# Performance work log

Measured on AMD Instinct MI355X. Metric: run time of the kernel, lower is better.

## Reference

```python
import jax, jax.numpy as jnp
import numpy as np

N_NODES = 100000
N_EDGES = 1200000
D = 64
N_LAYERS = 3


def setup_inputs() -> dict:
    key = jax.random.key(0)
    k0, k1, k2, k3, k4 = jax.random.split(key, 5)
    x = jax.random.normal(k0, (N_NODES, D), dtype=jnp.float32)
    edge_index = jax.random.randint(k1, (2, N_EDGES), 0, N_NODES, dtype=jnp.int32)
    edge_weight = jax.random.uniform(k2, (N_EDGES,), dtype=jnp.float32)
    # stacked per-layer params: 3 layers of 64->64
    self_kernels = jax.random.normal(k3, (N_LAYERS, D, D), dtype=jnp.float32) * 0.1
    neighbor_kernels = jax.random.normal(k4, (N_LAYERS, D, D), dtype=jnp.float32) * 0.1
    biases = jnp.zeros((N_LAYERS, D), dtype=jnp.float32)
    return {"x": x, "edge_index": edge_index, "edge_weight": edge_weight,
            "self_kernels": self_kernels, "neighbor_kernels": neighbor_kernels,
            "biases": biases}


def _sage_layer(h, row, col, edge_weight, self_k, neigh_k, b):
    # gather source-node features per edge, weight them: [E, d]
    msg = h[col] * edge_weight[:, None]
    # sum-aggregate messages at target nodes: [N, d]
    agg = jax.ops.segment_sum(msg, row, num_segments=N_NODES)
    # concat=False -> self transform + neighbor transform added, then relu
    out = h @ self_k + agg @ neigh_k + b
    return jax.nn.relu(out)


def reference(x, edge_index, edge_weight, self_kernels, neighbor_kernels, biases):
    row, col = edge_index[0], edge_index[1]
    h = x
    for i in range(N_LAYERS):
        h = _sage_layer(h, row, col, edge_weight,
                        self_kernels[i], neighbor_kernels[i], biases[i])
    return h
```

## Files before the change

kernel.cpp:

```cpp
#include <hip/hip_runtime.h>

#define NN 100000
#define NE 1200000
#define DD 64
#define NTILES 3125
#define NBK 391
#define MLEN (NBK * 256)
#define EPB 4688

typedef unsigned int uint32;
typedef unsigned char uint8;
typedef unsigned short ushort16;
typedef __attribute__((ext_vector_type(8))) short short8;
typedef __attribute__((ext_vector_type(16))) float f32x16;

__device__ __forceinline__ ushort16 f2bf(float x) {
    uint32 u = __float_as_uint(x);
    u += 0x7FFFu + ((u >> 16) & 1u);
    return (ushort16)(u >> 16);
}
__device__ __forceinline__ float bflo(uint32 u) { return __uint_as_float(u << 16); }
__device__ __forceinline__ float bfhi(uint32 u) { return __uint_as_float(u & 0xFFFF0000u); }
__device__ __forceinline__ uint32 pack2(float a, float b) {
    return (uint32)f2bf(a) | ((uint32)f2bf(b) << 16);
}

__device__ __forceinline__ void agg_edges8(float* a, int s, int e, int fl,
                                           const uint32* __restrict__ edges,
                                           const uint4* __restrict__ y4) {
    #pragma unroll 4
    for (int j = s; j < e; j++) {
        uint32 ed = edges[j];
        int c = (int)(ed >> 15);
        float w = (float)(ed & 32767u) * (1.0f / 32767.0f);
        uint4 yv = y4[c * 8 + fl];
        a[0] = fmaf(bflo(yv.x), w, a[0]);
        a[1] = fmaf(bfhi(yv.x), w, a[1]);
        a[2] = fmaf(bflo(yv.y), w, a[2]);
        a[3] = fmaf(bfhi(yv.y), w, a[3]);
        a[4] = fmaf(bflo(yv.z), w, a[4]);
        a[5] = fmaf(bfhi(yv.z), w, a[5]);
        a[6] = fmaf(bflo(yv.w), w, a[6]);
        a[7] = fmaf(bfhi(yv.w), w, a[7]);
    }
}


__global__ __launch_bounds__(512)
void k_init(const int* __restrict__ row, int* __restrict__ M,
            const float* __restrict__ selfk, const float* __restrict__ neighk,
            short8* __restrict__ wpack) {
    if (blockIdx.x >= 256) {
        int tid = (blockIdx.x - 256) * 512 + threadIdx.x;
        if (tid < 3 * 16 * 64) {
            int lane  = tid & 63;
            int frag  = (tid >> 6) & 15;
            int layer = tid >> 10;
            int g = frag >> 3;
            int t = (frag >> 2) & 1;
            int s = frag & 3;
            const float* W = (g ? neighk : selfk) + layer * 4096;
            int n = t * 32 + (lane & 31);
            int k0 = s * 16 + (lane >> 5) * 8;
            short8 v;
            #pragma unroll
            for (int j = 0; j < 8; j++) v[j] = (short)f2bf(W[(k0 + j) * 64 + n]);
            wpack[tid] = v;
        }
        return;
    }
    __shared__ int bins[NBK];
    for (int i = threadIdx.x; i < NBK; i += 512) bins[i] = 0;
    __syncthreads();
    int start = blockIdx.x * EPB;
    int end = min(start + EPB, NE);
    for (int e = start + (int)threadIdx.x; e < end; e += 512)
        atomicAdd(&bins[row[e] >> 8], 1);
    __syncthreads();
    for (int i = threadIdx.x; i < NBK; i += 512)
        M[i * 256 + blockIdx.x] = bins[i];
}


__global__ void k_scan1(const int* __restrict__ in, int* __restrict__ outx,
                        int* __restrict__ partials) {
    __shared__ int tmp[256];
    int t = threadIdx.x;
    int i = blockIdx.x * 256 + t;
    int v = (i < MLEN) ? in[i] : 0;
    tmp[t] = v;
    __syncthreads();
    #pragma unroll
    for (int off = 1; off < 256; off <<= 1) {
        int add = (t >= off) ? tmp[t - off] : 0;
        __syncthreads();
        tmp[t] += add;
        __syncthreads();
    }
    if (i < MLEN) outx[i] = tmp[t] - v;
    if (t == 255) partials[blockIdx.x] = tmp[255];
}

__global__ void k_scan2(int* __restrict__ partials) {
    __shared__ int tmp[512];
    int t = threadIdx.x;
    int v = (t < NBK) ? partials[t] : 0;
    tmp[t] = v;
    __syncthreads();
    #pragma unroll
    for (int off = 1; off < 512; off <<= 1) {
        int add = (t >= off) ? tmp[t - off] : 0;
        __syncthreads();
        tmp[t] += add;
        __syncthreads();
    }
    if (t < NBK) partials[t] = tmp[t] - v;
}

__global__ __launch_bounds__(512)
void k_bscatter(const int* __restrict__ row, const int* __restrict__ col,
                const float* __restrict__ ew, const int* __restrict__ Mscan,
                const int* __restrict__ partials,
                uint32* __restrict__ colw, uint8* __restrict__ rowlo) {
    __shared__ int cur[NBK];
    for (int i = threadIdx.x; i < NBK; i += 512)
        cur[i] = Mscan[i * 256 + blockIdx.x] + partials[i];
    __syncthreads();
    int start = blockIdx.x * EPB;
    int end = min(start + EPB, NE);
    for (int e = start + (int)threadIdx.x; e < end; e += 512) {
        int r = row[e];
        int wq = (int)(ew[e] * 32767.0f + 0.5f);
        wq = (wq > 32767) ? 32767 : wq;
        int p = atomicAdd(&cur[r >> 8], 1);
        colw[p]  = ((uint32)col[e] << 15) | (uint32)wq;
        rowlo[p] = (uint8)(r & 255);
    }
}

__global__ __launch_bounds__(256)
void k_build(const int* __restrict__ Mscan, const int* __restrict__ partials,
             const uint32* __restrict__ colw, const uint8* __restrict__ rowlo,
             uint32* __restrict__ edges, int* __restrict__ offsets) {
    __shared__ int bins[256];
    __shared__ int tmp[256];
    __shared__ int cur[256];
    int b = blockIdx.x;
    int t = threadIdx.x;
    int bstart = Mscan[b * 256] + partials[b];
    int bend   = (b == NBK - 1) ? NE : Mscan[(b + 1) * 256] + partials[b + 1];
    bins[t] = 0;
    __syncthreads();
    for (int p = bstart + t; p < bend; p += 256)
        atomicAdd(&bins[rowlo[p]], 1);
    __syncthreads();
    int v = bins[t];
    tmp[t] = v;
    __syncthreads();
    #pragma unroll
    for (int off = 1; off < 256; off <<= 1) {
        int add = (t >= off) ? tmp[t - off] : 0;
        __syncthreads();
        tmp[t] += add;
        __syncthreads();
    }
    int base = bstart + (tmp[t] - v);
    cur[t] = base;
    int rowid = b * 256 + t;
    if (rowid < NN) offsets[rowid] = base;
    if (b == 0 && t == 0) offsets[NN] = NE;
    __syncthreads();
    for (int p = bstart + t; p < bend; p += 256) {
        uint32 cw = colw[p];
        int dst = atomicAdd(&cur[rowlo[p]], 1);
        edges[dst] = cw;
    }
}


__global__ __launch_bounds__(256)
void gemm_mfma(const float* __restrict__ hf_, ushort16* __restrict__ hs,
               ushort16* __restrict__ y,
               const short8* __restrict__ wpack,
               const float* __restrict__ bias) {
    int lane  = threadIdx.x & 63;
    int wave  = threadIdx.x >> 6;
    int wid   = blockIdx.x * 4 + wave;
    int nwv   = gridDim.x * 4;
    int mrow  = lane & 31;
    int khalf = lane >> 5;
    int t     = wid & 1;

    short8 Wf[2][4];
    #pragma unroll
    for (int g = 0; g < 2; g++)
        #pragma unroll
        for (int s = 0; s < 4; s++)
            Wf[g][s] = wpack[(((g * 2 + t) * 4) + s) * 64 + lane];

    float bval = bias[t * 32 + mrow];

    for (int tile = wid >> 1; tile < NTILES; tile += nwv >> 1) {
        int n0 = tile * 32;
        const float* hf = hf_ + (n0 + mrow) * 64 + khalf * 8;
        short8 A[4];
        #pragma unroll
        for (int s = 0; s < 4; s++) {
            short8 a;
            #pragma unroll
            for (int j = 0; j < 8; j++) a[j] = (short)f2bf(hf[s * 16 + j]);
            A[s] = a;
        }

        f32x16 acc0, acc1;
        #pragma unroll
        for (int r = 0; r < 16; r++) { acc0[r] = 0.f; acc1[r] = 0.f; }

        #pragma unroll
        for (int s = 0; s < 4; s++) {
            acc0 = __builtin_amdgcn_mfma_f32_32x32x16_bf16(A[s], Wf[0][s], acc0, 0, 0, 0);
            acc1 = __builtin_amdgcn_mfma_f32_32x32x16_bf16(A[s], Wf[1][s], acc1, 0, 0, 0);
        }

        int colbase = t * 32 + mrow;
        #pragma unroll
        for (int r = 0; r < 16; r++) {
            int rw = (r & 3) + 8 * (r >> 2) + 4 * khalf;
            int n = n0 + rw;
            hs[n * DD + colbase] = f2bf(acc0[r] + bval);
            y [n * DD + colbase] = f2bf(acc1[r]);
        }
    }
}


__global__ __launch_bounds__(256)
void agg_gemm(const uint4* __restrict__ hs4, const uint4* __restrict__ y4,
              ushort16* __restrict__ hs_out, ushort16* __restrict__ y_out,
              const int* __restrict__ offsets, const uint32* __restrict__ edges,
              const short8* __restrict__ wpack, const float* __restrict__ bias) {
    __shared__ uint32 sh[32 * 36];
    int lane = threadIdx.x & 63;
    int wave = threadIdx.x >> 6;
    int g  = lane >> 3;
    int fl = lane & 7;
    int n0 = blockIdx.x * 32;
    int lrow = wave * 8 + g;
    int n = n0 + lrow;

    uint4 hv = hs4[n * 8 + fl];
    float a[8] = {bflo(hv.x), bfhi(hv.x), bflo(hv.y), bfhi(hv.y),
                  bflo(hv.z), bfhi(hv.z), bflo(hv.w), bfhi(hv.w)};
    agg_edges8(a, offsets[n], offsets[n + 1], fl, edges, y4);

    uint32* dstp = &sh[lrow * 36 + fl * 4];
    dstp[0] = pack2(fmaxf(a[0], 0.f), fmaxf(a[1], 0.f));
    dstp[1] = pack2(fmaxf(a[2], 0.f), fmaxf(a[3], 0.f));
    dstp[2] = pack2(fmaxf(a[4], 0.f), fmaxf(a[5], 0.f));
    dstp[3] = pack2(fmaxf(a[6], 0.f), fmaxf(a[7], 0.f));
    __syncthreads();

    int mrow  = lane & 31;
    int khalf = lane >> 5;
    int gsel  = wave >> 1;
    int t     = wave & 1;

    short8 Wf[4];
    #pragma unroll
    for (int s = 0; s < 4; s++)
        Wf[s] = wpack[(((gsel * 2 + t) * 4) + s) * 64 + lane];

    short8 A[4];
    #pragma unroll
    for (int s = 0; s < 4; s++)
        A[s] = *(const short8*)&sh[mrow * 36 + s * 8 + khalf * 4];

    f32x16 acc;
    #pragma unroll
    for (int r = 0; r < 16; r++) acc[r] = 0.f;
    #pragma unroll
    for (int s = 0; s < 4; s++)
        acc = __builtin_amdgcn_mfma_f32_32x32x16_bf16(A[s], Wf[s], acc, 0, 0, 0);

    float bval = gsel ? 0.f : bias[t * 32 + mrow];
    ushort16* dst = gsel ? y_out : hs_out;
    int colbase = t * 32 + mrow;
    #pragma unroll
    for (int r = 0; r < 16; r++) {
        int rw = (r & 3) + 8 * (r >> 2) + 4 * khalf;
        int nn = n0 + rw;
        dst[nn * DD + colbase] = f2bf(acc[r] + bval);
    }
}


__global__ __launch_bounds__(256)
void agg_final(const uint4* __restrict__ hs4, const uint4* __restrict__ y4,
               float4* __restrict__ out, const int* __restrict__ offsets,
               const uint32* __restrict__ edges) {
    int lane = threadIdx.x & 63;
    int wave = threadIdx.x >> 6;
    int g  = lane >> 3;
    int fl = lane & 7;
    int n = blockIdx.x * 32 + wave * 8 + g;

    uint4 hv = hs4[n * 8 + fl];
    float a[8] = {bflo(hv.x), bfhi(hv.x), bflo(hv.y), bfhi(hv.y),
                  bflo(hv.z), bfhi(hv.z), bflo(hv.w), bfhi(hv.w)};
    agg_edges8(a, offsets[n], offsets[n + 1], fl, edges, y4);

    out[n * 16 + fl * 2]     = make_float4(fmaxf(a[0], 0.f), fmaxf(a[1], 0.f),
                                           fmaxf(a[2], 0.f), fmaxf(a[3], 0.f));
    out[n * 16 + fl * 2 + 1] = make_float4(fmaxf(a[4], 0.f), fmaxf(a[5], 0.f),
                                           fmaxf(a[6], 0.f), fmaxf(a[7], 0.f));
}


extern "C" void kernel_launch(void* const* d_in, const int* in_sizes, int n_in,
                              void* d_out, int out_size, void* d_ws, size_t ws_size,
                              hipStream_t stream) {
    const float* x      = (const float*)d_in[0];
    const int*   ei     = (const int*)d_in[1];
    const float* ew     = (const float*)d_in[2];
    const float* selfk  = (const float*)d_in[3];
    const float* neighk = (const float*)d_in[4];
    const float* biases = (const float*)d_in[5];
    float* out = (float*)d_out;

    char* w = (char*)d_ws;
    ushort16* hsA   = (ushort16*)w; w += (size_t)NN * DD * sizeof(ushort16);
    ushort16* yA    = (ushort16*)w; w += (size_t)NN * DD * sizeof(ushort16);
    ushort16* hsB   = (ushort16*)w; w += (size_t)NN * DD * sizeof(ushort16);
    ushort16* yB    = (ushort16*)w; w += (size_t)NN * DD * sizeof(ushort16);
    uint32* edges   = (uint32*)w;   w += (size_t)NE * sizeof(uint32);
    uint32* colwB   = (uint32*)w;   w += (size_t)NE * sizeof(uint32);
    uint8*  rowlo   = (uint8*)w;    w += (size_t)NE * sizeof(uint8);
    w = (char*)(((size_t)w + 255) & ~(size_t)255);
    int*    M       = (int*)w;      w += (size_t)MLEN * sizeof(int);
    int*    Mscan   = (int*)w;      w += (size_t)MLEN * sizeof(int);
    int*    offsets = (int*)w;      w += (size_t)(NN + 1) * sizeof(int);
    int*    partials= (int*)w;      w += 512 * sizeof(int);
    short8* wpack   = (short8*)w;   w += (size_t)3 * 16 * 64 * sizeof(short8);

    const int* row = ei;
    const int* col = ei + NE;

    k_init    <<<262, 512, 0, stream>>>(row, M, selfk, neighk, wpack);
    k_scan1   <<<NBK, 256, 0, stream>>>(M, Mscan, partials);
    k_scan2   <<<1, 512, 0, stream>>>(partials);
    k_bscatter<<<256, 512, 0, stream>>>(row, col, ew, Mscan, partials, colwB, rowlo);
    k_build   <<<NBK, 256, 0, stream>>>(Mscan, partials, colwB, rowlo, edges, offsets);

    gemm_mfma<<<782, 256, 0, stream>>>(x, hsA, yA, wpack, biases);
    agg_gemm <<<NTILES, 256, 0, stream>>>((const uint4*)hsA, (const uint4*)yA,
                                          hsB, yB, offsets, edges,
                                          wpack + 1024, biases + 64);
    agg_gemm <<<NTILES, 256, 0, stream>>>((const uint4*)hsB, (const uint4*)yB,
                                          hsA, yA, offsets, edges,
                                          wpack + 2048, biases + 128);
    agg_final<<<NTILES, 256, 0, stream>>>((const uint4*)hsA, (const uint4*)yA,
                                          (float4*)out, offsets, edges);
}
```

Before: 227.0 us.

## Fuse first GEMM into init, merge scan2 into bscatter, stage edges in LDS, fp32 y

Moves the layer-0 MFMA GEMM into extra blocks of the init kernel and folds the second-level scan into the bucket-scatter kernel, removing two launches. Per-tile edge lists are preloaded into shared memory with decoded byte offsets and float weights, with a global fallback past a fixed capacity. The neighbor-transformed features y are now stored as fp32 rather than bf16, which removes unpacking work but doubles gather traffic. The init kernel's GEMM blocks compute weights directly from fp32 kernels and overlap with the histogram work.

```diff
diff --git a/kernel.cpp b/kernel.cpp
--- a/kernel.cpp
+++ b/kernel.cpp
@@ -7,6 +7,7 @@
 #define NBK 391
 #define MLEN (NBK * 256)
 #define EPB 4688
+#define ECAP 768
 
 typedef unsigned int uint32;
 typedef unsigned char uint8;
@@ -25,23 +26,46 @@
     return (uint32)f2bf(a) | ((uint32)f2bf(b) << 16);
 }
 
-__device__ __forceinline__ void agg_edges8(float* a, int s, int e, int fl,
-                                           const uint32* __restrict__ edges,
-                                           const uint4* __restrict__ y4) {
+__device__ __forceinline__ void agg_lds(float* a, int ls, int le, uint32 flB,
+                                        const uint2* __restrict__ esh,
+                                        const char* __restrict__ ybase) {
     #pragma unroll 4
+    for (int j = ls; j < le; j++) {
+        uint2 ei = esh[j];
+        uint32 boff = ei.x + flB;
+        float w = __uint_as_float(ei.y);
+        const float4* p = (const float4*)(ybase + boff);
+        float4 y0 = p[0];
+        float4 y1 = p[1];
+        a[0] = fmaf(y0.x, w, a[0]);
+        a[1] = fmaf(y0.y, w, a[1]);
+        a[2] = fmaf(y0.z, w, a[2]);
+        a[3] = fmaf(y0.w, w, a[3]);
+        a[4] = fmaf(y1.x, w, a[4]);
+        a[5] = fmaf(y1.y, w, a[5]);
+        a[6] = fmaf(y1.z, w, a[6]);
+        a[7] = fmaf(y1.w, w, a[7]);
+    }
+}
+
+__device__ __forceinline__ void agg_glob(float* a, int s, int e, uint32 flB,
+                                         const uint32* __restrict__ edges,
+                                         const char* __restrict__ ybase) {
     for (int j = s; j < e; j++) {
         uint32 ed = edges[j];
-        int c = (int)(ed >> 15);
+        uint32 boff = ((ed >> 15) << 8) + flB;
         float w = (float)(ed & 32767u) * (1.0f / 32767.0f);
-        uint4 yv = y4[c * 8 + fl];
-        a[0] = fmaf(bflo(yv.x), w, a[0]);
-        a[1] = fmaf(bfhi(yv.x), w, a[1]);
-        a[2] = fmaf(bflo(yv.y), w, a[2]);
-        a[3] = fmaf(bfhi(yv.y), w, a[3]);
-        a[4] = fmaf(bflo(yv.z), w, a[4]);
-        a[5] = fmaf(bfhi(yv.z), w, a[5]);
-        a[6] = fmaf(bflo(yv.w), w, a[6]);
-        a[7] = fmaf(bfhi(yv.w), w, a[7]);
+        const float4* p = (const float4*)(ybase + boff);
+        float4 y0 = p[0];
+        float4 y1 = p[1];
+        a[0] = fmaf(y0.x, w, a[0]);
+        a[1] = fmaf(y0.y, w, a[1]);
+        a[2] = fmaf(y0.z, w, a[2]);
+        a[3] = fmaf(y0.w, w, a[3]);
+        a[4] = fmaf(y1.x, w, a[4]);
+        a[5] = fmaf(y1.y, w, a[5]);
+        a[6] = fmaf(y1.z, w, a[6]);
+        a[7] = fmaf(y1.w, w, a[7]);
     }
 }
 
@@ -49,7 +73,66 @@
 __global__ __launch_bounds__(512)
 void k_init(const int* __restrict__ row, int* __restrict__ M,
             const float* __restrict__ selfk, const float* __restrict__ neighk,
-            short8* __restrict__ wpack) {
+            short8* __restrict__ wpack, const float* __restrict__ x,
+            ushort16* __restrict__ hs, float* __restrict__ y,
+            const float* __restrict__ biases) {
+    if (blockIdx.x >= 262) {
+        int lane  = threadIdx.x & 63;
+        int wave  = threadIdx.x >> 6;
+        int wid   = (blockIdx.x - 262) * 8 + wave;
+        int mrow  = lane & 31;
+        int khalf = lane >> 5;
+        int t     = wid & 1;
+
+        short8 Wf[2][4];
+        #pragma unroll
+        for (int g = 0; g < 2; g++) {
+            const float* W = g ? neighk : selfk;
+            #pragma unroll
+            for (int s = 0; s < 4; s++) {
+                int k0 = s * 16 + khalf * 8;
+                short8 v;
+                #pragma unroll
+                for (int j = 0; j < 8; j++)
+                    v[j] = (short)f2bf(W[(k0 + j) * 64 + t * 32 + mrow]);
+                Wf[g][s] = v;
+            }
+        }
+        float bval = biases[t * 32 + mrow];
+
+        for (int tile = wid >> 1; tile < NTILES; tile += 1564) {
+            int n0 = tile * 32;
+            const float* hf = x + (n0 + mrow) * 64 + khalf * 8;
+            short8 A[4];
+            #pragma unroll
+            for (int s = 0; s < 4; s++) {
+                short8 a;
+                #pragma unroll
+                for (int j = 0; j < 8; j++) a[j] = (short)f2bf(hf[s * 16 + j]);
+                A[s] = a;
+            }
+
+            f32x16 acc0, acc1;
+            #pragma unroll
+            for (int r = 0; r < 16; r++) { acc0[r] = 0.f; acc1[r] = 0.f; }
+
+            #pragma unroll
+            for (int s = 0; s < 4; s++) {
+                acc0 = __builtin_amdgcn_mfma_f32_32x32x16_bf16(A[s], Wf[0][s], acc0, 0, 0, 0);
+                acc1 = __builtin_amdgcn_mfma_f32_32x32x16_bf16(A[s], Wf[1][s], acc1, 0, 0, 0);
+            }
+
+            int colbase = t * 32 + mrow;
+            #pragma unroll
+            for (int r = 0; r < 16; r++) {
+                int rw = (r & 3) + 8 * (r >> 2) + 4 * khalf;
+                int nn = n0 + rw;
+                hs[nn * DD + colbase] = f2bf(acc0[r] + bval);
+                y [nn * 64 + colbase] = acc1[r];
+            }
+        }
+        return;
+    }
     if (blockIdx.x >= 256) {
         int tid = (blockIdx.x - 256) * 512 + threadIdx.x;
         if (tid < 3 * 16 * 64) {
@@ -101,8 +184,13 @@
     if (t == 255) partials[blockIdx.x] = tmp[255];
 }
 
-__global__ void k_scan2(int* __restrict__ partials) {
+__global__ __launch_bounds__(512)
+void k_bscatter(const int* __restrict__ row, const int* __restrict__ col,
+                const float* __restrict__ ew, const int* __restrict__ Mscan,
+                const int* __restrict__ partials, int* __restrict__ partials2,
+                uint32* __restrict__ colw, uint8* __restrict__ rowlo) {
     __shared__ int tmp[512];
+    __shared__ int cur[NBK];
     int t = threadIdx.x;
     int v = (t < NBK) ? partials[t] : 0;
     tmp[t] = v;
@@ -114,17 +202,11 @@
         tmp[t] += add;
         __syncthreads();
     }
-    if (t < NBK) partials[t] = tmp[t] - v;
-}
-
-__global__ __launch_bounds__(512)
-void k_bscatter(const int* __restrict__ row, const int* __restrict__ col,
-                const float* __restrict__ ew, const int* __restrict__ Mscan,
-                const int* __restrict__ partials,
-                uint32* __restrict__ colw, uint8* __restrict__ rowlo) {
-    __shared__ int cur[NBK];
-    for (int i = threadIdx.x; i < NBK; i += 512)
-        cur[i] = Mscan[i * 256 + blockIdx.x] + partials[i];
+    if (t < NBK) {
+        int excl = tmp[t] - v;
+        cur[t] = Mscan[t * 256 + blockIdx.x] + excl;
+        if (blockIdx.x == 0) partials2[t] = excl;
+    }
     __syncthreads();
     int start = blockIdx.x * EPB;
     int end = min(start + EPB, NE);
@@ -139,7 +221,7 @@
 }
 
 __global__ __launch_bounds__(256)
-void k_build(const int* __restrict__ Mscan, const int* __restrict__ partials,
+void k_build(const int* __restrict__ Mscan, const int* __restrict__ partials2,
              const uint32* __restrict__ colw, const uint8* __restrict__ rowlo,
              uint32* __restrict__ edges, int* __restrict__ offsets) {
     __shared__ int bins[256];
@@ -147,8 +229,8 @@
     __shared__ int cur[256];
     int b = blockIdx.x;
     int t = threadIdx.x;
-    int bstart = Mscan[b * 256] + partials[b];
-    int bend   = (b == NBK - 1) ? NE : Mscan[(b + 1) * 256] + partials[b + 1];
+    int bstart = Mscan[b * 256] + partials2[b];
+    int bend   = (b == NBK - 1) ? NE : Mscan[(b + 1) * 256] + partials2[b + 1];
     bins[t] = 0;
     __syncthreads();
     for (int p = bstart + t; p < bend; p += 256)
@@ -179,67 +261,12 @@
 
 
 __global__ __launch_bounds__(256)
-void gemm_mfma(const float* __restrict__ hf_, ushort16* __restrict__ hs,
-               ushort16* __restrict__ y,
-               const short8* __restrict__ wpack,
-               const float* __restrict__ bias) {
-    int lane  = threadIdx.x & 63;
-    int wave  = threadIdx.x >> 6;
-    int wid   = blockIdx.x * 4 + wave;
-    int nwv   = gridDim.x * 4;
-    int mrow  = lane & 31;
-    int khalf = lane >> 5;
-    int t     = wid & 1;
-
-    short8 Wf[2][4];
-    #pragma unroll
-    for (int g = 0; g < 2; g++)
-        #pragma unroll
-        for (int s = 0; s < 4; s++)
-            Wf[g][s] = wpack[(((g * 2 + t) * 4) + s) * 64 + lane];
-
-    float bval = bias[t * 32 + mrow];
-
-    for (int tile = wid >> 1; tile < NTILES; tile += nwv >> 1) {
-        int n0 = tile * 32;
-        const float* hf = hf_ + (n0 + mrow) * 64 + khalf * 8;
-        short8 A[4];
-        #pragma unroll
-        for (int s = 0; s < 4; s++) {
-            short8 a;
-            #pragma unroll
-            for (int j = 0; j < 8; j++) a[j] = (short)f2bf(hf[s * 16 + j]);
-            A[s] = a;
-        }
-
-        f32x16 acc0, acc1;
-        #pragma unroll
-        for (int r = 0; r < 16; r++) { acc0[r] = 0.f; acc1[r] = 0.f; }
-
-        #pragma unroll
-        for (int s = 0; s < 4; s++) {
-            acc0 = __builtin_amdgcn_mfma_f32_32x32x16_bf16(A[s], Wf[0][s], acc0, 0, 0, 0);
-            acc1 = __builtin_amdgcn_mfma_f32_32x32x16_bf16(A[s], Wf[1][s], acc1, 0, 0, 0);
-        }
-
-        int colbase = t * 32 + mrow;
-        #pragma unroll
-        for (int r = 0; r < 16; r++) {
-            int rw = (r & 3) + 8 * (r >> 2) + 4 * khalf;
-            int n = n0 + rw;
-            hs[n * DD + colbase] = f2bf(acc0[r] + bval);
-            y [n * DD + colbase] = f2bf(acc1[r]);
-        }
-    }
-}
-
-
-__global__ __launch_bounds__(256)
-void agg_gemm(const uint4* __restrict__ hs4, const uint4* __restrict__ y4,
-              ushort16* __restrict__ hs_out, ushort16* __restrict__ y_out,
+void agg_gemm(const uint4* __restrict__ hs4, const float* __restrict__ yf,
+              ushort16* __restrict__ hs_out, float* __restrict__ y_out,
               const int* __restrict__ offsets, const uint32* __restrict__ edges,
               const short8* __restrict__ wpack, const float* __restrict__ bias) {
     __shared__ uint32 sh[32 * 36];
+    __shared__ uint2 esh[ECAP];
     int lane = threadIdx.x & 63;
     int wave = threadIdx.x >> 6;
     int g  = lane >> 3;
@@ -248,10 +275,26 @@
     int lrow = wave * 8 + g;
     int n = n0 + lrow;
 
+    int ebase = offsets[n0];
+    int m = min(offsets[n0 + 32] - ebase, ECAP);
+    for (int i = threadIdx.x; i < m; i += 256) {
+        uint32 ed = edges[ebase + i];
+        esh[i] = make_uint2((ed >> 15) << 8,
+                            __float_as_uint((float)(ed & 32767u) * (1.0f / 32767.0f)));
+    }
+    int s = offsets[n];
+    int e = offsets[n + 1];
     uint4 hv = hs4[n * 8 + fl];
+    __syncthreads();
+
     float a[8] = {bflo(hv.x), bfhi(hv.x), bflo(hv.y), bfhi(hv.y),
                   bflo(hv.z), bfhi(hv.z), bflo(hv.w), bfhi(hv.w)};
-    agg_edges8(a, offsets[n], offsets[n + 1], fl, edges, y4);
+    uint32 flB = (uint32)fl * 32u;
+    const char* ybase = (const char*)yf;
+    int ls = s - ebase, le = e - ebase;
+    agg_lds(a, min(ls, ECAP), min(le, ECAP), flB, esh, ybase);
+    if (le > ECAP)
+        agg_glob(a, ebase + max(ls, ECAP), ebase + le, flB, edges, ybase);
 
     uint32* dstp = &sh[lrow * 36 + fl * 4];
     dstp[0] = pack2(fmaxf(a[0], 0.f), fmaxf(a[1], 0.f));
@@ -267,47 +310,71 @@
 
     short8 Wf[4];
     #pragma unroll
-    for (int s = 0; s < 4; s++)
-        Wf[s] = wpack[(((gsel * 2 + t) * 4) + s) * 64 + lane];
+    for (int ss = 0; ss < 4; ss++)
+        Wf[ss] = wpack[(((gsel * 2 + t) * 4) + ss) * 64 + lane];
 
     short8 A[4];
     #pragma unroll
-    for (int s = 0; s < 4; s++)
-        A[s] = *(const short8*)&sh[mrow * 36 + s * 8 + khalf * 4];
+    for (int ss = 0; ss < 4; ss++)
+        A[ss] = *(const short8*)&sh[mrow * 36 + ss * 8 + khalf * 4];
 
     f32x16 acc;
     #pragma unroll
     for (int r = 0; r < 16; r++) acc[r] = 0.f;
     #pragma unroll
-    for (int s = 0; s < 4; s++)
-        acc = __builtin_amdgcn_mfma_f32_32x32x16_bf16(A[s], Wf[s], acc, 0, 0, 0);
-
-    float bval = gsel ? 0.f : bias[t * 32 + mrow];
-    ushort16* dst = gsel ? y_out : hs_out;
+    for (int ss = 0; ss < 4; ss++)
+        acc = __builtin_amdgcn_mfma_f32_32x32x16_bf16(A[ss], Wf[ss], acc, 0, 0, 0);
+
     int colbase = t * 32 + mrow;
-    #pragma unroll
-    for (int r = 0; r < 16; r++) {
-        int rw = (r & 3) + 8 * (r >> 2) + 4 * khalf;
-        int nn = n0 + rw;
-        dst[nn * DD + colbase] = f2bf(acc[r] + bval);
+    if (gsel) {
+        #pragma unroll
+        for (int r = 0; r < 16; r++) {
+            int rw = (r & 3) + 8 * (r >> 2) + 4 * khalf;
+            y_out[(n0 + rw) * 64 + colbase] = acc[r];
+        }
+    } else {
+        float bval = bias[t * 32 + mrow];
+        #pragma unroll
+        for (int r = 0; r < 16; r++) {
+            int rw = (r & 3) + 8 * (r >> 2) + 4 * khalf;
+            hs_out[(n0 + rw) * DD + colbase] = f2bf(acc[r] + bval);
+        }
     }
 }
 
 
 __global__ __launch_bounds__(256)
-void agg_final(const uint4* __restrict__ hs4, const uint4* __restrict__ y4,
+void agg_final(const uint4* __restrict__ hs4, const float* __restrict__ yf,
                float4* __restrict__ out, const int* __restrict__ offsets,
                const uint32* __restrict__ edges) {
+    __shared__ uint2 esh[ECAP];
     int lane = threadIdx.x & 63;
     int wave = threadIdx.x >> 6;
     int g  = lane >> 3;
     int fl = lane & 7;
-    int n = blockIdx.x * 32 + wave * 8 + g;
-
+    int n0 = blockIdx.x * 32;
+    int n = n0 + wave * 8 + g;
+
+    int ebase = offsets[n0];
+    int m = min(offsets[n0 + 32] - ebase, ECAP);
+    for (int i = threadIdx.x; i < m; i += 256) {
+        uint32 ed = edges[ebase + i];
+        esh[i] = make_uint2((ed >> 15) << 8,
+                            __float_as_uint((float)(ed & 32767u) * (1.0f / 32767.0f)));
+    }
+    int s = offsets[n];
+    int e = offsets[n + 1];
     uint4 hv = hs4[n * 8 + fl];
+    __syncthreads();
+
     float a[8] = {bflo(hv.x), bfhi(hv.x), bflo(hv.y), bfhi(hv.y),
                   bflo(hv.z), bfhi(hv.z), bflo(hv.w), bfhi(hv.w)};
-    agg_edges8(a, offsets[n], offsets[n + 1], fl, edges, y4);
+    uint32 flB = (uint32)fl * 32u;
+    const char* ybase = (const char*)yf;
+    int ls = s - ebase, le = e - ebase;
+    agg_lds(a, min(ls, ECAP), min(le, ECAP), flB, esh, ybase);
+    if (le > ECAP)
+        agg_glob(a, ebase + max(ls, ECAP), ebase + le, flB, edges, ybase);
 
     out[n * 16 + fl * 2]     = make_float4(fmaxf(a[0], 0.f), fmaxf(a[1], 0.f),
                                            fmaxf(a[2], 0.f), fmaxf(a[3], 0.f));
@@ -329,9 +396,9 @@
 
     char* w = (char*)d_ws;
     ushort16* hsA   = (ushort16*)w; w += (size_t)NN * DD * sizeof(ushort16);
-    ushort16* yA    = (ushort16*)w; w += (size_t)NN * DD * sizeof(ushort16);
+    float*    yA    = (float*)w;    w += (size_t)NN * DD * sizeof(float);
     ushort16* hsB   = (ushort16*)w; w += (size_t)NN * DD * sizeof(ushort16);
-    ushort16* yB    = (ushort16*)w; w += (size_t)NN * DD * sizeof(ushort16);
+    float*    yB    = (float*)w;    w += (size_t)NN * DD * sizeof(float);
     uint32* edges   = (uint32*)w;   w += (size_t)NE * sizeof(uint32);
     uint32* colwB   = (uint32*)w;   w += (size_t)NE * sizeof(uint32);
     uint8*  rowlo   = (uint8*)w;    w += (size_t)NE * sizeof(uint8);
@@ -340,24 +407,25 @@
     int*    Mscan   = (int*)w;      w += (size_t)MLEN * sizeof(int);
     int*    offsets = (int*)w;      w += (size_t)(NN + 1) * sizeof(int);
     int*    partials= (int*)w;      w += 512 * sizeof(int);
+    int*    partials2=(int*)w;      w += 512 * sizeof(int);
     short8* wpack   = (short8*)w;   w += (size_t)3 * 16 * 64 * sizeof(short8);
 
     const int* row = ei;
     const int* col = ei + NE;
 
-    k_init    <<<262, 512, 0, stream>>>(row, M, selfk, neighk, wpack);
+    k_init    <<<653, 512, 0, stream>>>(row, M, selfk, neighk, wpack,
+                                        x, hsA, yA, biases);
     k_scan1   <<<NBK, 256, 0, stream>>>(M, Mscan, partials);
-    k_scan2   <<<1, 512, 0, stream>>>(partials);
-    k_bscatter<<<256, 512, 0, stream>>>(row, col, ew, Mscan, partials, colwB, rowlo);
-    k_build   <<<NBK, 256, 0, stream>>>(Mscan, partials, colwB, rowlo, edges, offsets);
-
-    gemm_mfma<<<782, 256, 0, stream>>>(x, hsA, yA, wpack, biases);
-    agg_gemm <<<NTILES, 256, 0, stream>>>((const uint4*)hsA, (const uint4*)yA,
+    k_bscatter<<<256, 512, 0, stream>>>(row, col, ew, Mscan, partials, partials2,
+                                        colwB, rowlo);
+    k_build   <<<NBK, 256, 0, stream>>>(Mscan, partials2, colwB, rowlo, edges, offsets);
+
+    agg_gemm <<<NTILES, 256, 0, stream>>>((const uint4*)hsA, yA,
                                           hsB, yB, offsets, edges,
                                           wpack + 1024, biases + 64);
-    agg_gemm <<<NTILES, 256, 0, stream>>>((const uint4*)hsB, (const uint4*)yB,
+    agg_gemm <<<NTILES, 256, 0, stream>>>((const uint4*)hsB, yB,
                                           hsA, yA, offsets, edges,
                                           wpack + 2048, biases + 128);
-    agg_final<<<NTILES, 256, 0, stream>>>((const uint4*)hsA, (const uint4*)yA,
+    agg_final<<<NTILES, 256, 0, stream>>>((const uint4*)hsA, yA,
                                           (float4*)out, offsets, edges);
 }
```

Result: slower. 272.3 us (+19.9%).
